# Kernel optimization log

Measured on AMD Instinct MI355X. Metric: run time of the kernel, lower is better.

The kernel has to match this reference:

```python
import jax, jax.numpy as jnp
import numpy as np

INPUT_SIZE = 1024
HIDDEN_SIZE = 1024
LN_EPS = 1e-5


def setup_inputs() -> dict:
    key = jax.random.key(0)
    ks = jax.random.split(key, 8)
    bs, n = 4, 2048
    # Xavier-uniform bound for square (in=out) linear layers
    bound = float(np.sqrt(6.0 / (INPUT_SIZE + HIDDEN_SIZE)))
    x = jax.random.normal(ks[0], (bs, n, INPUT_SIZE), dtype=jnp.float32)
    wq = jax.random.uniform(ks[1], (INPUT_SIZE, HIDDEN_SIZE), jnp.float32, -bound, bound)
    wk = jax.random.uniform(ks[2], (INPUT_SIZE, HIDDEN_SIZE), jnp.float32, -bound, bound)
    wv = jax.random.uniform(ks[3], (INPUT_SIZE, HIDDEN_SIZE), jnp.float32, -bound, bound)
    bq = jnp.zeros((HIDDEN_SIZE,), jnp.float32)
    bk = jnp.zeros((HIDDEN_SIZE,), jnp.float32)
    bv = jnp.zeros((HIDDEN_SIZE,), jnp.float32)
    ln_w = jnp.ones((INPUT_SIZE,), jnp.float32)
    ln_b = jnp.zeros((INPUT_SIZE,), jnp.float32)
    return {"x": x, "wq": wq, "bq": bq, "wk": wk, "bk": bk,
            "wv": wv, "bv": bv, "ln_w": ln_w, "ln_b": ln_b}


def _layernorm(x, w, b):
    mu = jnp.mean(x, axis=-1, keepdims=True)
    var = jnp.mean(jnp.square(x - mu), axis=-1, keepdims=True)
    return (x - mu) * jax.lax.rsqrt(var + LN_EPS) * w + b


def reference(x, wq, bq, wk, bk, wv, bv, ln_w, ln_b):
    # x: [b, n, d_in]
    xn = _layernorm(x, ln_w, ln_b)
    q = jnp.einsum('bnd,dh->bnh', xn, wq) + bq
    k = jnp.einsum('bnd,dh->bnh', xn, wk) + bk
    v = jnp.einsum('bnd,dh->bnh', xn, wv) + bv
    scale = 1.0 / np.sqrt(HIDDEN_SIZE)
    att = jnp.einsum('bqh,bkh->bqk', q, k) * scale  # [b, n, n]
    att = jax.nn.softmax(att, axis=-1)
    out = jnp.einsum('bqk,bkh->bqh', att, v)  # [b, n, h]
    return (att, out)
```

## Files before the change

### kernel.cpp

```cpp
#include <hip/hip_runtime.h>
#include <stdint.h>


typedef __attribute__((ext_vector_type(8))) short short8;
typedef __attribute__((ext_vector_type(4))) float floatx4;
typedef __attribute__((ext_vector_type(4))) uint16_t u16x4;

__device__ __forceinline__ uint16_t f2bf(float f) {
    union { float f; uint32_t u; } v; v.f = f;
    uint32_t r = v.u + 0x7fffu + ((v.u >> 16) & 1u);
    return (uint16_t)(r >> 16);
}

typedef const uint32_t __attribute__((address_space(1)))* gas1_t;
typedef uint32_t __attribute__((address_space(3)))* las3_t;
__device__ __forceinline__ void gload_lds16(const uint16_t* g, uint16_t* l) {
    __builtin_amdgcn_global_load_lds((gas1_t)g, (las3_t)l, 16, 0, 0);
}

__device__ __forceinline__ void s_bar()  { asm volatile("s_barrier" ::: "memory"); }
__device__ __forceinline__ void lgkm0()  { asm volatile("s_waitcnt lgkmcnt(0)" ::: "memory"); }
template<int N> __device__ __forceinline__ void vmw() {
    asm volatile("s_waitcnt vmcnt(%0)" :: "n"(N) : "memory");
}


#define READS(BASE, KS)                                                   \
    { const uint16_t* LBp = (BASE) + ABUF;                                \
      _Pragma("unroll") for (int mi = 0; mi < 8; ++mi)                    \
          Af[mi][KS] = *(const short8*)((BASE) + aoff + mi * 1024 +       \
                                        ((KS) ? ksg1 : ksg0));            \
      _Pragma("unroll") for (int ni = 0; ni < NIW; ++ni)                  \
          Bf[ni][KS] = *(const short8*)(LBp + boff + ni * 1024 +          \
                                        ((KS) ? ksg1 : ksg0)); }

#define MFMAS(KS)                                                         \
    __builtin_amdgcn_s_setprio(1);                                        \
    _Pragma("unroll") for (int mi = 0; mi < 8; ++mi)                      \
    _Pragma("unroll") for (int ni = 0; ni < NIW; ++ni)                    \
        acc[mi][ni] = __builtin_amdgcn_mfma_f32_16x16x32_bf16(            \
            Af[mi][KS], Bf[ni][KS], acc[mi][ni], 0, 0, 0);                \
    __builtin_amdgcn_s_setprio(0);

template<int BN, int EPI>
__device__ __forceinline__ void gemm_fat(
    const uint16_t* __restrict__ A, const uint16_t* __restrict__ Bt,
    const int K, const int NT, const int m0, const int n0,
    float* __restrict__ Cf, uint16_t* __restrict__ Cb, const int ldc,
    const float* __restrict__ bq, const float* __restrict__ bk,
    const float* __restrict__ bv, const float alpha)
{
    constexpr int ABUF  = 16384;
    constexpr int BP    = BN / 32;
    constexpr int BBUF  = BN * 64;
    constexpr int BUFSZ = ABUF + BBUF;
    constexpr int OPS   = 8 + BP;
    constexpr int NIW   = BN / 32;
    __shared__ uint16_t sm[2 * BUFSZ + 2048];
    uint16_t* const trash = sm + 2 * BUFSZ;

    const int t = threadIdx.x;

    const int srow = t >> 3;
    const int sseg = (t & 7) ^ (srow & 7);
    const uint16_t* gA = A + (size_t)(m0 + srow) * K + sseg * 8;
    const uint16_t* gB = Bt + (size_t)(n0 + srow) * K + sseg * 8;

    auto STGALL = [&](int kt, int b) {
        const bool lv = kt < NT;
        const size_t ko = (size_t)(lv ? kt : 0) * 64;
        uint16_t* const db = sm + b * BUFSZ + t * 8;
        uint16_t* const tr = trash + t * 8;
#pragma unroll
        for (int p = 0; p < 8; ++p)
            gload_lds16(gA + (size_t)(p * 32) * K + ko,
                        lv ? (db + p * 2048) : tr);
#pragma unroll
        for (int p = 0; p < BP; ++p)
            gload_lds16(gB + (size_t)(p * 32) * K + ko,
                        lv ? (db + ABUF + p * 2048) : tr);
    };

    const int lane = t & 63;
    const int wid  = t >> 6;
    const int wm   = wid >> 1;
    const int wn   = wid & 1;
    const int quad = lane >> 4;
    const int lrow = lane & 15;
    const int swz  = lrow & 7;
    const int ksg0 = (quad ^ swz) * 8;
    const int ksg1 = ((4 + quad) ^ swz) * 8;
    const int aoff = (wm * 128 + lrow) * 64;
    const int boff = (wn * (16 * NIW) + lrow) * 64;

    floatx4 acc[8][NIW];
#pragma unroll
    for (int mi = 0; mi < 8; ++mi)
#pragma unroll
        for (int ni = 0; ni < NIW; ++ni)
            acc[mi][ni] = floatx4{0.f, 0.f, 0.f, 0.f};

    short8 Af[8][2];
    short8 Bf[NIW][2];

    STGALL(0, 0);
    STGALL(1, 1);
    vmw<OPS>();
    s_bar();
    READS(sm, 0);

    for (int te = 0; te < NT; ++te) {
        const uint16_t* LA  = sm + (te & 1) * BUFSZ;
        const uint16_t* LAn = sm + ((te + 1) & 1) * BUFSZ;

        READS(LA, 1);
        MFMAS(0);
        lgkm0();
        s_bar();
        STGALL(te + 2, te & 1);
        vmw<OPS>();
        s_bar();
        READS(LAn, 0);
        MFMAS(1);
    }

    vmw<0>();

    const int rbase = m0 + wm * 128 + quad * 4;
    const int cbase = n0 + wn * (16 * NIW) + lrow;

    if constexpr (EPI == 1) {
        float bc[NIW];
#pragma unroll
        for (int ni = 0; ni < NIW; ++ni) {
            const int col = cbase + ni * 16;
            const int z = col >> 10;
            const float* bp = (z == 0) ? bq : ((z == 1) ? bk : bv);
            bc[ni] = bp[col & 1023];
        }
#pragma unroll
        for (int mi = 0; mi < 8; ++mi) {
#pragma unroll
            for (int ni = 0; ni < NIW; ++ni) {
                const int row = rbase + mi * 16;
                const int col = cbase + ni * 16;
                const int z = col >> 10, h = col & 1023;
#pragma unroll
                for (int r = 0; r < 4; ++r)
                    Cb[(size_t)z * 8388608 + (size_t)(row + r) * 1024 + h] =
                        f2bf(acc[mi][ni][r] + bc[ni]);
            }
        }
    } else {
#pragma unroll
        for (int mi = 0; mi < 8; ++mi) {
#pragma unroll
            for (int ni = 0; ni < NIW; ++ni) {
                const int row = rbase + mi * 16;
                const int col = cbase + ni * 16;
#pragma unroll
                for (int r = 0; r < 4; ++r)
                    Cf[(size_t)(row + r) * ldc + col] = acc[mi][ni][r] * alpha;
            }
        }
    }
}

__global__ __launch_bounds__(256, 1) void k_qkv(
    const uint16_t* __restrict__ xn, const uint16_t* __restrict__ wt,
    const float* __restrict__ bq, const float* __restrict__ bk,
    const float* __restrict__ bv, uint16_t* __restrict__ qkv)
{
    const int flat = blockIdx.y * 16 + blockIdx.x;
    const int s = (flat & 7) * 64 + (flat >> 3);
    const int bx = s & 15, by = s >> 4;
    gemm_fat<192, 1>(xn, wt, 1024, 16, by * 256, bx * 192,
                     nullptr, qkv, 0, bq, bk, bv, 0.f);
}

__global__ __launch_bounds__(256, 1) void k_scores(
    const uint16_t* __restrict__ q, const uint16_t* __restrict__ k,
    float* __restrict__ S)
{
    const int flat = (blockIdx.z * 8 + blockIdx.y) * 16 + blockIdx.x;
    const int s = (flat & 7) * 64 + (flat >> 3);
    const int x = s & 15, y = (s >> 4) & 7, z = s >> 7;
    gemm_fat<128, 0>(q + (size_t)z * 2048 * 1024, k + (size_t)z * 2048 * 1024,
                     1024, 16, y * 256, x * 128,
                     S + (size_t)z * 2048 * 2048, nullptr, 2048,
                     nullptr, nullptr, nullptr, 0.03125f);
}

__global__ __launch_bounds__(256, 1) void k_out(
    const uint16_t* __restrict__ attb, const uint16_t* __restrict__ vt,
    float* __restrict__ out)
{
    const int flat = blockIdx.z * 64 + blockIdx.y * 8 + blockIdx.x;
    const int s = (flat & 7) * 32 + (flat >> 3);
    const int z = s >> 6, y = (s >> 3) & 7, x = s & 7;
    gemm_fat<128, 0>(attb + (size_t)z * 2048 * 2048, vt + (size_t)z * 1024 * 2048,
                     2048, 32, y * 256, x * 128,
                     out + (size_t)z * 2048 * 1024, nullptr, 1024,
                     nullptr, nullptr, nullptr, 1.0f);
}

__global__ __launch_bounds__(256) void k_ln(
    const float* __restrict__ x, const float* __restrict__ lw,
    const float* __restrict__ lb, uint16_t* __restrict__ xn)
{
    const int row = blockIdx.x;
    const int t = threadIdx.x;
    const float* xr = x + (size_t)row * 1024;
    const float4 xv = ((const float4*)xr)[t];
    float s  = xv.x + xv.y + xv.z + xv.w;
    float s2 = xv.x * xv.x + xv.y * xv.y + xv.z * xv.z + xv.w * xv.w;
#pragma unroll
    for (int off = 32; off > 0; off >>= 1) {
        s  += __shfl_xor(s, off);
        s2 += __shfl_xor(s2, off);
    }
    __shared__ float ps[4], ps2[4];
    const int w = t >> 6, lane = t & 63;
    if (lane == 0) { ps[w] = s; ps2[w] = s2; }
    __syncthreads();
    s  = ps[0] + ps[1] + ps[2] + ps[3];
    s2 = ps2[0] + ps2[1] + ps2[2] + ps2[3];
    const float mu  = s * (1.f / 1024.f);
    const float var = s2 * (1.f / 1024.f) - mu * mu;
    const float rs  = rsqrtf(var + 1e-5f);
    const float4 wv = ((const float4*)lw)[t];
    const float4 bv = ((const float4*)lb)[t];
    u16x4 o;
    o.x = f2bf((xv.x - mu) * rs * wv.x + bv.x);
    o.y = f2bf((xv.y - mu) * rs * wv.y + bv.y);
    o.z = f2bf((xv.z - mu) * rs * wv.z + bv.z);
    o.w = f2bf((xv.w - mu) * rs * wv.w + bv.w);
    ((u16x4*)(xn + (size_t)row * 1024))[t] = o;
}

__global__ void k_wt(const float* __restrict__ wq, const float* __restrict__ wk,
                     const float* __restrict__ wv, uint16_t* __restrict__ wt)
{
    __shared__ float tile[32][33];
    const int z = blockIdx.z;
    const float* W = (z == 0) ? wq : ((z == 1) ? wk : wv);
    uint16_t* T = wt + (size_t)z * 1024 * 1024;
    const int c0 = blockIdx.x * 32, r0 = blockIdx.y * 32;
    const int tx = threadIdx.x, ty = threadIdx.y;
#pragma unroll
    for (int i = 0; i < 4; i++)
        tile[ty + 8 * i][tx] = W[(size_t)(r0 + ty + 8 * i) * 1024 + c0 + tx];
    __syncthreads();
#pragma unroll
    for (int i = 0; i < 4; i++)
        T[(size_t)(c0 + ty + 8 * i) * 1024 + r0 + tx] = f2bf(tile[tx][ty + 8 * i]);
}

__global__ __launch_bounds__(256) void k_vt(
    const uint16_t* __restrict__ v, uint16_t* __restrict__ vt)
{
    __shared__ uint16_t tile[64][68];
    const int b = blockIdx.z;
    const uint16_t* V = v + (size_t)b * 2048 * 1024;
    uint16_t* T = vt + (size_t)b * 1024 * 2048;
    const int h0 = blockIdx.x * 64, t0 = blockIdx.y * 64;
    const int t = threadIdx.x;
    const int rr = t >> 4;
    const int cc = (t & 15) * 4;
#pragma unroll
    for (int i = 0; i < 4; i++) {
        const int tok = rr + 16 * i;
        *(u16x4*)&tile[tok][cc] =
            *(const u16x4*)&V[(size_t)(t0 + tok) * 1024 + h0 + cc];
    }
    __syncthreads();
#pragma unroll
    for (int i = 0; i < 4; i++) {
        const int h = rr + 16 * i;
        u16x4 o;
        o.x = tile[cc + 0][h];
        o.y = tile[cc + 1][h];
        o.z = tile[cc + 2][h];
        o.w = tile[cc + 3][h];
        *(u16x4*)&T[(size_t)(h0 + h) * 2048 + t0 + cc] = o;
    }
}

__global__ __launch_bounds__(256) void k_softmax(
    float* __restrict__ S, uint16_t* __restrict__ attb)
{
    const size_t row = blockIdx.x;
    float* p = S + row * 2048;
    const int t = threadIdx.x;
    float4 a = ((float4*)p)[2 * t];
    float4 b = ((float4*)p)[2 * t + 1];
    float m = fmaxf(fmaxf(fmaxf(a.x, a.y), fmaxf(a.z, a.w)),
                    fmaxf(fmaxf(b.x, b.y), fmaxf(b.z, b.w)));
#pragma unroll
    for (int off = 32; off > 0; off >>= 1) m = fmaxf(m, __shfl_xor(m, off));
    __shared__ float pm[4], pl[4];
    const int w = t >> 6, lane = t & 63;
    if (lane == 0) pm[w] = m;
    __syncthreads();
    m = fmaxf(fmaxf(pm[0], pm[1]), fmaxf(pm[2], pm[3]));

    a.x = __expf(a.x - m); a.y = __expf(a.y - m);
    a.z = __expf(a.z - m); a.w = __expf(a.w - m);
    b.x = __expf(b.x - m); b.y = __expf(b.y - m);
    b.z = __expf(b.z - m); b.w = __expf(b.w - m);
    float s = a.x + a.y + a.z + a.w + b.x + b.y + b.z + b.w;
#pragma unroll
    for (int off = 32; off > 0; off >>= 1) s += __shfl_xor(s, off);
    if (lane == 0) pl[w] = s;
    __syncthreads();
    s = pl[0] + pl[1] + pl[2] + pl[3];
    const float inv = 1.f / s;

    a.x *= inv; a.y *= inv; a.z *= inv; a.w *= inv;
    b.x *= inv; b.y *= inv; b.z *= inv; b.w *= inv;
    ((float4*)p)[2 * t]     = a;
    ((float4*)p)[2 * t + 1] = b;

    uint16_t* q = attb + row * 2048 + t * 8;
    u16x4 o0, o1;
    o0.x = f2bf(a.x); o0.y = f2bf(a.y); o0.z = f2bf(a.z); o0.w = f2bf(a.w);
    o1.x = f2bf(b.x); o1.y = f2bf(b.y); o1.z = f2bf(b.z); o1.w = f2bf(b.w);
    ((u16x4*)q)[0] = o0;
    ((u16x4*)q)[1] = o1;
}

extern "C" void kernel_launch(void* const* d_in, const int* in_sizes, int n_in,
                              void* d_out, int out_size, void* d_ws, size_t ws_size,
                              hipStream_t stream)
{
    const float* x  = (const float*)d_in[0];
    const float* wq = (const float*)d_in[1];
    const float* bq = (const float*)d_in[2];
    const float* wk = (const float*)d_in[3];
    const float* bk = (const float*)d_in[4];
    const float* wv = (const float*)d_in[5];
    const float* bv = (const float*)d_in[6];
    const float* lw = (const float*)d_in[7];
    const float* lb = (const float*)d_in[8];

    float* att = (float*)d_out;
    float* out = (float*)d_out + (size_t)16777216;

    uint16_t* xn = (uint16_t*)d_out;
    uint16_t* wt = (uint16_t*)d_out + (size_t)8388608;

    uint16_t* ws   = (uint16_t*)d_ws;
    uint16_t* q    = ws;
    uint16_t* k    = ws + (size_t)8388608;
    uint16_t* v    = ws + (size_t)2 * 8388608;
    uint16_t* vt   = ws;
    uint16_t* attb = ws + (size_t)8388608;
    uint16_t* qkv  = q;

    if (ws_size < (size_t)50331648) return;

    k_ln<<<8192, 256, 0, stream>>>(x, lw, lb, xn);
    k_wt<<<dim3(32, 32, 3), dim3(32, 8), 0, stream>>>(wq, wk, wv, wt);
    k_qkv<<<dim3(16, 32), 256, 0, stream>>>(xn, wt, bq, bk, bv, qkv);
    k_scores<<<dim3(16, 8, 4), 256, 0, stream>>>(q, k, att);
    k_vt<<<dim3(16, 32, 4), 256, 0, stream>>>(v, vt);
    k_softmax<<<8192, 256, 0, stream>>>(att, attb);
    k_out<<<dim3(8, 8, 4), 256, 0, stream>>>(attb, vt, out);
}
```

Before: 335.7 us.

## Shrink GEMM tiles to 128x128, load B fragments directly from global, fuse prep kernels

The GEMM core moves from 256-row fat tiles (single block per CU) to 128x128 tiles. Only the A operand is staged through LDS; B fragments are read straight from global memory into registers, and launch bounds are raised to allow up to four blocks per CU. The grids grow to match, giving more blocks for occupancy and latency hiding, at the cost of less operand reuse per tile and uncached, non-LDS B loads inside the loop. The layernorm and weight-transpose kernels are also merged into a single launch.

New measurement: 676.6 us. 2.02x slower.

```diff
diff --git a/kernel.cpp b/kernel.cpp
--- a/kernel.cpp
+++ b/kernel.cpp
@@ -25,60 +25,49 @@
 }
 
 
-#define READS(BASE, KS)                                                   \
-    { const uint16_t* LBp = (BASE) + ABUF;                                \
-      _Pragma("unroll") for (int mi = 0; mi < 8; ++mi)                    \
-          Af[mi][KS] = *(const short8*)((BASE) + aoff + mi * 1024 +       \
-                                        ((KS) ? ksg1 : ksg0));            \
-      _Pragma("unroll") for (int ni = 0; ni < NIW; ++ni)                  \
-          Bf[ni][KS] = *(const short8*)(LBp + boff + ni * 1024 +          \
-                                        ((KS) ? ksg1 : ksg0)); }
-
+#define READSA(BASE, KS)                                                  \
+    _Pragma("unroll") for (int mi = 0; mi < 4; ++mi)                      \
+        Af[mi][KS] = *(const short8*)((BASE) + aoff + mi * 1024 +         \
+                                      ((KS) ? ksg1 : ksg0));
+#define LOADB(TE, KS)                                                     \
+    _Pragma("unroll") for (int ni = 0; ni < 4; ++ni)                      \
+        Bf[ni][KS] = *(const short8*)(gBf + (size_t)(ni * 16) * K +       \
+                                      (size_t)(TE) * 64 + (KS) * 32);
 #define MFMAS(KS)                                                         \
     __builtin_amdgcn_s_setprio(1);                                        \
-    _Pragma("unroll") for (int mi = 0; mi < 8; ++mi)                      \
-    _Pragma("unroll") for (int ni = 0; ni < NIW; ++ni)                    \
+    _Pragma("unroll") for (int mi = 0; mi < 4; ++mi)                      \
+    _Pragma("unroll") for (int ni = 0; ni < 4; ++ni)                      \
         acc[mi][ni] = __builtin_amdgcn_mfma_f32_16x16x32_bf16(            \
             Af[mi][KS], Bf[ni][KS], acc[mi][ni], 0, 0, 0);                \
     __builtin_amdgcn_s_setprio(0);
 
-template<int BN, int EPI>
-__device__ __forceinline__ void gemm_fat(
+template<int EPI>
+__device__ __forceinline__ void gemm_bd(
     const uint16_t* __restrict__ A, const uint16_t* __restrict__ Bt,
     const int K, const int NT, const int m0, const int n0,
     float* __restrict__ Cf, uint16_t* __restrict__ Cb, const int ldc,
     const float* __restrict__ bq, const float* __restrict__ bk,
     const float* __restrict__ bv, const float alpha)
 {
-    constexpr int ABUF  = 16384;
-    constexpr int BP    = BN / 32;
-    constexpr int BBUF  = BN * 64;
-    constexpr int BUFSZ = ABUF + BBUF;
-    constexpr int OPS   = 8 + BP;
-    constexpr int NIW   = BN / 32;
-    __shared__ uint16_t sm[2 * BUFSZ + 2048];
-    uint16_t* const trash = sm + 2 * BUFSZ;
+    constexpr int ABUF = 128 * 64;
+    __shared__ uint16_t sm[2 * ABUF + 2048];
+    uint16_t* const trash = sm + 2 * ABUF;
 
     const int t = threadIdx.x;
 
     const int srow = t >> 3;
     const int sseg = (t & 7) ^ (srow & 7);
     const uint16_t* gA = A + (size_t)(m0 + srow) * K + sseg * 8;
-    const uint16_t* gB = Bt + (size_t)(n0 + srow) * K + sseg * 8;
-
-    auto STGALL = [&](int kt, int b) {
+
+    auto STGA = [&](int kt, int b) {
         const bool lv = kt < NT;
         const size_t ko = (size_t)(lv ? kt : 0) * 64;
-        uint16_t* const db = sm + b * BUFSZ + t * 8;
+        uint16_t* const db = sm + b * ABUF + t * 8;
         uint16_t* const tr = trash + t * 8;
 #pragma unroll
-        for (int p = 0; p < 8; ++p)
+        for (int p = 0; p < 4; ++p)
             gload_lds16(gA + (size_t)(p * 32) * K + ko,
                         lv ? (db + p * 2048) : tr);
-#pragma unroll
-        for (int p = 0; p < BP; ++p)
-            gload_lds16(gB + (size_t)(p * 32) * K + ko,
-                        lv ? (db + ABUF + p * 2048) : tr);
     };
 
     const int lane = t & 63;
@@ -90,58 +79,62 @@
     const int swz  = lrow & 7;
     const int ksg0 = (quad ^ swz) * 8;
     const int ksg1 = ((4 + quad) ^ swz) * 8;
-    const int aoff = (wm * 128 + lrow) * 64;
-    const int boff = (wn * (16 * NIW) + lrow) * 64;
-
-    floatx4 acc[8][NIW];
-#pragma unroll
-    for (int mi = 0; mi < 8; ++mi)
-#pragma unroll
-        for (int ni = 0; ni < NIW; ++ni)
+    const int aoff = (wm * 64 + lrow) * 64;
+
+    const uint16_t* gBf = Bt + (size_t)(n0 + wn * 64 + lrow) * K + quad * 8;
+
+    floatx4 acc[4][4];
+#pragma unroll
+    for (int mi = 0; mi < 4; ++mi)
+#pragma unroll
+        for (int ni = 0; ni < 4; ++ni)
             acc[mi][ni] = floatx4{0.f, 0.f, 0.f, 0.f};
 
-    short8 Af[8][2];
-    short8 Bf[NIW][2];
-
-    STGALL(0, 0);
-    STGALL(1, 1);
-    vmw<OPS>();
+    short8 Af[4][2];
+    short8 Bf[4][2];
+
+    STGA(0, 0);
+    STGA(1, 1);
+    vmw<4>();
     s_bar();
-    READS(sm, 0);
+    READSA(sm, 0)
+    LOADB(0, 0)
 
     for (int te = 0; te < NT; ++te) {
-        const uint16_t* LA  = sm + (te & 1) * BUFSZ;
-        const uint16_t* LAn = sm + ((te + 1) & 1) * BUFSZ;
-
-        READS(LA, 1);
-        MFMAS(0);
+        const uint16_t* LA  = sm + (te & 1) * ABUF;
+        const uint16_t* LAn = sm + ((te + 1) & 1) * ABUF;
+
+        READSA(LA, 1)
+        LOADB(te, 1)
+        MFMAS(0)
         lgkm0();
         s_bar();
-        STGALL(te + 2, te & 1);
-        vmw<OPS>();
+        STGA(te + 2, te & 1);
+        vmw<4>();
         s_bar();
-        READS(LAn, 0);
-        MFMAS(1);
+        READSA(LAn, 0)
+        LOADB(te + 1, 0)
+        MFMAS(1)
     }
 
     vmw<0>();
 
-    const int rbase = m0 + wm * 128 + quad * 4;
-    const int cbase = n0 + wn * (16 * NIW) + lrow;
+    const int rbase = m0 + wm * 64 + quad * 4;
+    const int cbase = n0 + wn * 64 + lrow;
 
     if constexpr (EPI == 1) {
-        float bc[NIW];
-#pragma unroll
-        for (int ni = 0; ni < NIW; ++ni) {
+        float bc[4];
+#pragma unroll
+        for (int ni = 0; ni < 4; ++ni) {
             const int col = cbase + ni * 16;
             const int z = col >> 10;
             const float* bp = (z == 0) ? bq : ((z == 1) ? bk : bv);
             bc[ni] = bp[col & 1023];
         }
 #pragma unroll
-        for (int mi = 0; mi < 8; ++mi) {
-#pragma unroll
-            for (int ni = 0; ni < NIW; ++ni) {
+        for (int mi = 0; mi < 4; ++mi) {
+#pragma unroll
+            for (int ni = 0; ni < 4; ++ni) {
                 const int row = rbase + mi * 16;
                 const int col = cbase + ni * 16;
                 const int z = col >> 10, h = col & 1023;
@@ -153,9 +146,9 @@
         }
     } else {
 #pragma unroll
-        for (int mi = 0; mi < 8; ++mi) {
-#pragma unroll
-            for (int ni = 0; ni < NIW; ++ni) {
+        for (int mi = 0; mi < 4; ++mi) {
+#pragma unroll
+            for (int ni = 0; ni < 4; ++ni) {
                 const int row = rbase + mi * 16;
                 const int col = cbase + ni * 16;
 #pragma unroll
@@ -166,94 +159,96 @@
     }
 }
 
-__global__ __launch_bounds__(256, 1) void k_qkv(
+__global__ __launch_bounds__(256, 4) void k_qkv(
     const uint16_t* __restrict__ xn, const uint16_t* __restrict__ wt,
     const float* __restrict__ bq, const float* __restrict__ bk,
     const float* __restrict__ bv, uint16_t* __restrict__ qkv)
 {
-    const int flat = blockIdx.y * 16 + blockIdx.x;
-    const int s = (flat & 7) * 64 + (flat >> 3);
-    const int bx = s & 15, by = s >> 4;
-    gemm_fat<192, 1>(xn, wt, 1024, 16, by * 256, bx * 192,
-                     nullptr, qkv, 0, bq, bk, bv, 0.f);
-}
-
-__global__ __launch_bounds__(256, 1) void k_scores(
+    const int flat = blockIdx.y * 24 + blockIdx.x;
+    const int s = (flat & 7) * 192 + (flat >> 3);
+    const int bx = s % 24, by = s / 24;
+    gemm_bd<1>(xn, wt, 1024, 16, by * 128, bx * 128,
+               nullptr, qkv, 0, bq, bk, bv, 0.f);
+}
+
+__global__ __launch_bounds__(256, 4) void k_scores(
     const uint16_t* __restrict__ q, const uint16_t* __restrict__ k,
     float* __restrict__ S)
 {
-    const int flat = (blockIdx.z * 8 + blockIdx.y) * 16 + blockIdx.x;
-    const int s = (flat & 7) * 64 + (flat >> 3);
-    const int x = s & 15, y = (s >> 4) & 7, z = s >> 7;
-    gemm_fat<128, 0>(q + (size_t)z * 2048 * 1024, k + (size_t)z * 2048 * 1024,
-                     1024, 16, y * 256, x * 128,
-                     S + (size_t)z * 2048 * 2048, nullptr, 2048,
-                     nullptr, nullptr, nullptr, 0.03125f);
-}
-
-__global__ __launch_bounds__(256, 1) void k_out(
+    const int flat = (blockIdx.z * 16 + blockIdx.y) * 16 + blockIdx.x;
+    const int s = (flat & 7) * 128 + (flat >> 3);
+    const int x = s & 15, y = (s >> 4) & 15, z = s >> 8;
+    gemm_bd<0>(q + (size_t)z * 2048 * 1024, k + (size_t)z * 2048 * 1024,
+               1024, 16, y * 128, x * 128,
+               S + (size_t)z * 2048 * 2048, nullptr, 2048,
+               nullptr, nullptr, nullptr, 0.03125f);
+}
+
+__global__ __launch_bounds__(256, 4) void k_out(
     const uint16_t* __restrict__ attb, const uint16_t* __restrict__ vt,
     float* __restrict__ out)
 {
-    const int flat = blockIdx.z * 64 + blockIdx.y * 8 + blockIdx.x;
-    const int s = (flat & 7) * 32 + (flat >> 3);
-    const int z = s >> 6, y = (s >> 3) & 7, x = s & 7;
-    gemm_fat<128, 0>(attb + (size_t)z * 2048 * 2048, vt + (size_t)z * 1024 * 2048,
-                     2048, 32, y * 256, x * 128,
-                     out + (size_t)z * 2048 * 1024, nullptr, 1024,
-                     nullptr, nullptr, nullptr, 1.0f);
-}
-
-__global__ __launch_bounds__(256) void k_ln(
+    const int flat = (blockIdx.z * 16 + blockIdx.y) * 8 + blockIdx.x;
+    const int s = (flat & 7) * 64 + (flat >> 3);
+    const int x = s & 7, y = (s >> 3) & 15, z = s >> 7;
+    gemm_bd<0>(attb + (size_t)z * 2048 * 2048, vt + (size_t)z * 1024 * 2048,
+               2048, 32, y * 128, x * 128,
+               out + (size_t)z * 2048 * 1024, nullptr, 1024,
+               nullptr, nullptr, nullptr, 1.0f);
+}
+
+__global__ __launch_bounds__(256) void k_prep(
     const float* __restrict__ x, const float* __restrict__ lw,
-    const float* __restrict__ lb, uint16_t* __restrict__ xn)
-{
-    const int row = blockIdx.x;
+    const float* __restrict__ lb, uint16_t* __restrict__ xn,
+    const float* __restrict__ wq, const float* __restrict__ wk,
+    const float* __restrict__ wv, uint16_t* __restrict__ wt)
+{
     const int t = threadIdx.x;
-    const float* xr = x + (size_t)row * 1024;
-    const float4 xv = ((const float4*)xr)[t];
-    float s  = xv.x + xv.y + xv.z + xv.w;
-    float s2 = xv.x * xv.x + xv.y * xv.y + xv.z * xv.z + xv.w * xv.w;
-#pragma unroll
-    for (int off = 32; off > 0; off >>= 1) {
-        s  += __shfl_xor(s, off);
-        s2 += __shfl_xor(s2, off);
-    }
-    __shared__ float ps[4], ps2[4];
-    const int w = t >> 6, lane = t & 63;
-    if (lane == 0) { ps[w] = s; ps2[w] = s2; }
-    __syncthreads();
-    s  = ps[0] + ps[1] + ps[2] + ps[3];
-    s2 = ps2[0] + ps2[1] + ps2[2] + ps2[3];
-    const float mu  = s * (1.f / 1024.f);
-    const float var = s2 * (1.f / 1024.f) - mu * mu;
-    const float rs  = rsqrtf(var + 1e-5f);
-    const float4 wv = ((const float4*)lw)[t];
-    const float4 bv = ((const float4*)lb)[t];
-    u16x4 o;
-    o.x = f2bf((xv.x - mu) * rs * wv.x + bv.x);
-    o.y = f2bf((xv.y - mu) * rs * wv.y + bv.y);
-    o.z = f2bf((xv.z - mu) * rs * wv.z + bv.z);
-    o.w = f2bf((xv.w - mu) * rs * wv.w + bv.w);
-    ((u16x4*)(xn + (size_t)row * 1024))[t] = o;
-}
-
-__global__ void k_wt(const float* __restrict__ wq, const float* __restrict__ wk,
-                     const float* __restrict__ wv, uint16_t* __restrict__ wt)
-{
-    __shared__ float tile[32][33];
-    const int z = blockIdx.z;
-    const float* W = (z == 0) ? wq : ((z == 1) ? wk : wv);
-    uint16_t* T = wt + (size_t)z * 1024 * 1024;
-    const int c0 = blockIdx.x * 32, r0 = blockIdx.y * 32;
-    const int tx = threadIdx.x, ty = threadIdx.y;
-#pragma unroll
-    for (int i = 0; i < 4; i++)
-        tile[ty + 8 * i][tx] = W[(size_t)(r0 + ty + 8 * i) * 1024 + c0 + tx];
-    __syncthreads();
-#pragma unroll
-    for (int i = 0; i < 4; i++)
-        T[(size_t)(c0 + ty + 8 * i) * 1024 + r0 + tx] = f2bf(tile[tx][ty + 8 * i]);
+    if (blockIdx.x < 8192) {
+        const int row = blockIdx.x;
+        const float* xr = x + (size_t)row * 1024;
+        const float4 xv = ((const float4*)xr)[t];
+        float s  = xv.x + xv.y + xv.z + xv.w;
+        float s2 = xv.x * xv.x + xv.y * xv.y + xv.z * xv.z + xv.w * xv.w;
+#pragma unroll
+        for (int off = 32; off > 0; off >>= 1) {
+            s  += __shfl_xor(s, off);
+            s2 += __shfl_xor(s2, off);
+        }
+        __shared__ float ps[4], ps2[4];
+        const int w = t >> 6, lane = t & 63;
+        if (lane == 0) { ps[w] = s; ps2[w] = s2; }
+        __syncthreads();
+        s  = ps[0] + ps[1] + ps[2] + ps[3];
+        s2 = ps2[0] + ps2[1] + ps2[2] + ps2[3];
+        const float mu  = s * (1.f / 1024.f);
+        const float var = s2 * (1.f / 1024.f) - mu * mu;
+        const float rs  = rsqrtf(var + 1e-5f);
+        const float4 wv4 = ((const float4*)lw)[t];
+        const float4 bv4 = ((const float4*)lb)[t];
+        u16x4 o;
+        o.x = f2bf((xv.x - mu) * rs * wv4.x + bv4.x);
+        o.y = f2bf((xv.y - mu) * rs * wv4.y + bv4.y);
+        o.z = f2bf((xv.z - mu) * rs * wv4.z + bv4.z);
+        o.w = f2bf((xv.w - mu) * rs * wv4.w + bv4.w);
+        ((u16x4*)(xn + (size_t)row * 1024))[t] = o;
+    } else {
+        __shared__ float tile[32][33];
+        const int bid = blockIdx.x - 8192;
+        const int z = bid >> 10;
+        const int rem = bid & 1023;
+        const int c0 = (rem & 31) * 32, r0 = (rem >> 5) * 32;
+        const float* W = (z == 0) ? wq : ((z == 1) ? wk : wv);
+        uint16_t* T = wt + (size_t)z * 1024 * 1024;
+        const int tx = t & 31, ty = t >> 5;
+#pragma unroll
+        for (int i = 0; i < 4; i++)
+            tile[ty + 8 * i][tx] = W[(size_t)(r0 + ty + 8 * i) * 1024 + c0 + tx];
+        __syncthreads();
+#pragma unroll
+        for (int i = 0; i < 4; i++)
+            T[(size_t)(c0 + ty + 8 * i) * 1024 + r0 + tx] = f2bf(tile[tx][ty + 8 * i]);
+    }
 }
 
 __global__ __launch_bounds__(256) void k_vt(
@@ -359,11 +354,10 @@
 
     if (ws_size < (size_t)50331648) return;
 
-    k_ln<<<8192, 256, 0, stream>>>(x, lw, lb, xn);
-    k_wt<<<dim3(32, 32, 3), dim3(32, 8), 0, stream>>>(wq, wk, wv, wt);
-    k_qkv<<<dim3(16, 32), 256, 0, stream>>>(xn, wt, bq, bk, bv, qkv);
-    k_scores<<<dim3(16, 8, 4), 256, 0, stream>>>(q, k, att);
+    k_prep<<<8192 + 3072, 256, 0, stream>>>(x, lw, lb, xn, wq, wk, wv, wt);
+    k_qkv<<<dim3(24, 64), 256, 0, stream>>>(xn, wt, bq, bk, bv, qkv);
+    k_scores<<<dim3(16, 16, 4), 256, 0, stream>>>(q, k, att);
     k_vt<<<dim3(16, 32, 4), 256, 0, stream>>>(v, vt);
     k_softmax<<<8192, 256, 0, stream>>>(att, attb);
-    k_out<<<dim3(8, 8, 4), 256, 0, stream>>>(attb, vt, out);
-}
+    k_out<<<dim3(8, 16, 4), 256, 0, stream>>>(attb, vt, out);
+}
```
